# Kernel optimization log

Hardware: AMD Instinct MI355X
Metric: run time of the kernel (lower is better)

## Reference

```python
import jax, jax.numpy as jnp
import numpy as np

# Static block configuration (HTSAT stage-1 Swin block)
H = W = 64      # input_resolution
WS = 8          # window_size
SS = 4          # shift_size (window_size // 2)
NH = 4          # num_heads
C = 96          # dim
N = WS * WS     # tokens per window


def _rel_pos_index(ws):
    # mirrors WindowAttention.__init__ relative_position_index construction
    coords = np.stack(np.meshgrid(np.arange(ws), np.arange(ws), indexing='ij')).reshape(2, -1)
    rel = (coords[:, :, None] - coords[:, None, :]).transpose(1, 2, 0)
    rel[:, :, 0] += ws - 1
    rel[:, :, 1] += ws - 1
    rel[:, :, 0] *= 2 * ws - 1
    return rel.sum(-1)  # (N, N) int


def _attn_mask(h, w, ws, ss):
    # mirrors SwinTransformerBlock shifted-window attn_mask construction
    img = np.zeros((h, w))
    slices = (slice(0, -ws), slice(-ws, -ss), slice(-ss, None))
    cnt = 0
    for hs in slices:
        for wsl in slices:
            img[hs, wsl] = cnt
            cnt += 1
    mw = img.reshape(h // ws, ws, w // ws, ws).transpose(0, 2, 1, 3).reshape(-1, ws * ws)
    diff = mw[:, None, :] - mw[:, :, None]  # (nW, N, N)
    return np.where(diff != 0, -100.0, 0.0).astype(np.float32)


_REL_IDX = jnp.asarray(_rel_pos_index(WS))          # (N, N)
_ATTN_MASK = jnp.asarray(_attn_mask(H, W, WS, SS))  # (nW, N, N)


def _layernorm(x, g, b, eps=1e-5):
    mu = x.mean(-1, keepdims=True)
    var = ((x - mu) ** 2).mean(-1, keepdims=True)
    return (x - mu) * jax.lax.rsqrt(var + eps) * g + b


def setup_inputs() -> dict:
    key = jax.random.key(0)
    ks = jax.random.split(key, 6)
    B = 64
    std = 0.02
    return {
        'x': jax.random.normal(ks[0], (B, H * W, C), jnp.float32),
        'norm1_g': jnp.ones((C,), jnp.float32),
        'norm1_b': jnp.zeros((C,), jnp.float32),
        'qkv_w': jax.random.normal(ks[1], (3 * C, C), jnp.float32) * std,
        'qkv_b': jnp.zeros((3 * C,), jnp.float32),
        'rpb_table': jax.random.normal(ks[2], ((2 * WS - 1) ** 2, NH), jnp.float32) * std,
        'proj_w': jax.random.normal(ks[3], (C, C), jnp.float32) * std,
        'proj_b': jnp.zeros((C,), jnp.float32),
        'norm2_g': jnp.ones((C,), jnp.float32),
        'norm2_b': jnp.zeros((C,), jnp.float32),
        'fc1_w': jax.random.normal(ks[4], (4 * C, C), jnp.float32) * std,
        'fc1_b': jnp.zeros((4 * C,), jnp.float32),
        'fc2_w': jax.random.normal(ks[5], (C, 4 * C), jnp.float32) * std,
        'fc2_b': jnp.zeros((C,), jnp.float32),
    }


def reference(x, norm1_g, norm1_b, qkv_w, qkv_b, rpb_table, proj_w, proj_b,
              norm2_g, norm2_b, fc1_w, fc1_b, fc2_w, fc2_b):
    B, L, _ = x.shape
    hd = C // NH
    scale = hd ** (-0.5)

    shortcut = x
    h = _layernorm(x, norm1_g, norm1_b).reshape(B, H, W, C)
    # cyclic shift
    h = jnp.roll(h, (-SS, -SS), axis=(1, 2))
    # window partition -> (B*nW, N, C)
    hw = h.reshape(B, H // WS, WS, W // WS, WS, C).transpose(0, 1, 3, 2, 4, 5).reshape(-1, N, C)
    B_ = hw.shape[0]

    qkv = (hw @ qkv_w.T + qkv_b).reshape(B_, N, 3, NH, hd).transpose(2, 0, 3, 1, 4)
    q, k, v = qkv[0], qkv[1], qkv[2]  # (B_, NH, N, hd)

    attn = jnp.einsum('bhnd,bhmd->bhnm', q * scale, k)
    bias = rpb_table[_REL_IDX.reshape(-1)].reshape(N, N, NH).transpose(2, 0, 1)
    attn = attn + bias[None]
    nW = _ATTN_MASK.shape[0]
    attn = attn.reshape(B_ // nW, nW, NH, N, N) + _ATTN_MASK[None, :, None]
    attn = jax.nn.softmax(attn.reshape(B_, NH, N, N), axis=-1)

    o = jnp.einsum('bhnm,bhmd->bhnd', attn, v).transpose(0, 2, 1, 3).reshape(B_, N, C)
    o = o @ proj_w.T + proj_b
    # window reverse
    o = o.reshape(B, H // WS, W // WS, WS, WS, C).transpose(0, 1, 3, 2, 4, 5).reshape(B, H, W, C)
    o = jnp.roll(o, (SS, SS), axis=(1, 2))

    x = shortcut + o.reshape(B, L, C)
    h2 = _layernorm(x, norm2_g, norm2_b)
    h2 = jax.nn.gelu(h2 @ fc1_w.T + fc1_b, approximate=False) @ fc2_w.T + fc2_b
    return x + h2
```

## Files before the change

### kernel.cpp

```cpp
#include <hip/hip_runtime.h>
#include <math.h>

#define B_IMG 64
#define H_ 64
#define W_ 64
#define L_ (H_*W_)
#define C_ 96
#define WSZ 8
#define SSZ 4
#define NH_ 4
#define HD_ 24
#define NT_ 64

#define QKVW_OFF 0
#define PROJW_OFF 27648
#define W1_OFF   36864
#define W2_OFF   73728
#define WTOT     110592

typedef short bf16x8 __attribute__((ext_vector_type(8)));
typedef float f32x4  __attribute__((ext_vector_type(4)));

__device__ __forceinline__ float bf2f(unsigned short u) {
    union { unsigned int i; float f; } c; c.i = ((unsigned int)u) << 16; return c.f;
}
__device__ __forceinline__ unsigned short f2bf(float f) {
    union { float f; unsigned int i; } c; c.f = f;
    return (unsigned short)((c.i + 0x7fffu + ((c.i >> 16) & 1u)) >> 16);
}
__device__ __forceinline__ int reg_of(int ii, int jj, int whi, int wwi) {
    const int rh = (whi == 7) ? ((ii < SSZ) ? 1 : 2) : 0;
    const int rw = (wwi == 7) ? ((jj < SSZ) ? 1 : 2) : 0;
    return rh*3 + rw;
}

__global__ void k_conv(const float* __restrict__ qkvw, const float* __restrict__ projw,
                       const float* __restrict__ w1, const float* __restrict__ w2,
                       unsigned short* __restrict__ ws16) {
    int i = blockIdx.x * 256 + threadIdx.x;
    if (i >= WTOT) return;
    float v;
    if (i < PROJW_OFF)      v = qkvw[i];
    else if (i < W1_OFF)    v = projw[i - PROJW_OFF];
    else if (i < W2_OFF)    v = w1[i - W1_OFF];
    else                    v = w2[i - W2_OFF];
    ws16[i] = f2bf(v);
}

__global__ __launch_bounds__(256)
void k_attn(const float* __restrict__ x,
            const float* __restrict__ g1, const float* __restrict__ b1,
            const unsigned short* __restrict__ wsw,
            const float* __restrict__ qkvb,
            const float* __restrict__ rpbt,
            const float* __restrict__ projb,
            float* __restrict__ xmid)
{
    const int wid = blockIdx.x;
    const int b = wid >> 6, whi = (wid >> 3) & 7, wwi = wid & 7;
    const int tid = threadIdx.x;
    const int l = tid & 63, wv = tid >> 6;
    const int e = l & 15, g = l >> 4;

    __shared__ __align__(16) unsigned short hbn[NT_][104];
    __shared__ __align__(16) unsigned short qkps[NH_][4096];
    __shared__ __align__(16) unsigned short vt[NH_][2048];
    __shared__ float rpbf[900];

    {
        uint4* z = (uint4*)&qkps[0][0];
        for (int i = tid; i < 2048; i += 256) z[i] = (uint4){0,0,0,0};
        for (int i = tid; i < 900; i += 256) rpbf[i] = rpbt[i];
    }

    {
        const int tok = tid >> 2, q = tid & 3;
        const int i = tok >> 3, j = tok & 7;
        const int sr = (whi*WSZ + i + SSZ) & (H_-1);
        const int sc = (wwi*WSZ + j + SSZ) & (W_-1);
        const float* row = x + ((size_t)b*L_ + sr*W_ + sc) * C_;
        float v[24];
        float s = 0.f, s2 = 0.f;
#pragma unroll
        for (int m = 0; m < 6; ++m) {
            float4 f = ((const float4*)row)[q + 4*m];
            v[4*m+0]=f.x; v[4*m+1]=f.y; v[4*m+2]=f.z; v[4*m+3]=f.w;
            s  += f.x+f.y+f.z+f.w;
            s2 += f.x*f.x+f.y*f.y+f.z*f.z+f.w*f.w;
        }
        s  += __shfl_xor(s, 1);  s  += __shfl_xor(s, 2);
        s2 += __shfl_xor(s2, 1); s2 += __shfl_xor(s2, 2);
        const float mu = s * (1.f/96.f);
        const float rstd = rsqrtf(s2*(1.f/96.f) - mu*mu + 1e-5f);
#pragma unroll
        for (int m = 0; m < 6; ++m) {
            const int c0 = 4*(q + 4*m);
            float o0 = (v[4*m+0]-mu)*rstd*g1[c0+0] + b1[c0+0];
            float o1 = (v[4*m+1]-mu)*rstd*g1[c0+1] + b1[c0+1];
            float o2 = (v[4*m+2]-mu)*rstd*g1[c0+2] + b1[c0+2];
            float o3 = (v[4*m+3]-mu)*rstd*g1[c0+3] + b1[c0+3];
            uint2 u;
            u.x = (unsigned int)f2bf(o0) | ((unsigned int)f2bf(o1) << 16);
            u.y = (unsigned int)f2bf(o2) | ((unsigned int)f2bf(o3) << 16);
            *(uint2*)&hbn[tok][c0] = u;
        }
    }
    __syncthreads();

    {
        f32x4 acc[18];
#pragma unroll
        for (int nt = 0; nt < 18; ++nt) acc[nt] = (f32x4){0.f,0.f,0.f,0.f};
#pragma unroll
        for (int ks = 0; ks < 3; ++ks) {
            bf16x8 a = *(const bf16x8*)&hbn[wv*16 + e][ks*32 + g*8];
#pragma unroll
            for (int nt = 0; nt < 18; ++nt) {
                bf16x8 bw = *(const bf16x8*)(wsw + QKVW_OFF + (size_t)(nt*16 + e)*96 + ks*32 + g*8);
                acc[nt] = __builtin_amdgcn_mfma_f32_16x16x32_bf16(a, bw, acc[nt], 0, 0, 0);
            }
        }
#pragma unroll
        for (int nt = 0; nt < 18; ++nt) {
            const int col = nt*16 + e;
            const int seg = nt / 6;
            const int cs  = col - seg*96;
            const int hh  = cs / 24;
            const int dd  = cs - hh*24;
            const float bias = qkvb[col];
#pragma unroll
            for (int i = 0; i < 4; ++i) {
                const int row = wv*16 + g*4 + i;
                const float val = acc[nt][i] + bias;
                if (seg == 0)      qkps[hh][row*32 + dd] = f2bf(val * 0.20412414523193154f);
                else if (seg == 1) qkps[hh][2048 + row*32 + dd] = f2bf(val);
                else               vt[hh][dd*64 + ((((row*2) ^ ((dd&7)<<4))) >> 1)] = f2bf(val);
            }
        }
    }
    __syncthreads();

    {
        const int hd = wv;
        const unsigned short* qbase = &qkps[hd][0];
        const unsigned short* kbase = &qkps[hd][2048];
        unsigned short* psb = &qkps[hd][0];

        f32x4 acc[4][4];
        {
            bf16x8 qf[4], kf[4];
#pragma unroll
            for (int mt = 0; mt < 4; ++mt)
                qf[mt] = *(const bf16x8*)(qbase + (mt*16 + e)*32 + g*8);
#pragma unroll
            for (int nt = 0; nt < 4; ++nt)
                kf[nt] = *(const bf16x8*)(kbase + (nt*16 + e)*32 + g*8);
            const f32x4 zz = (f32x4){0.f,0.f,0.f,0.f};
#pragma unroll
            for (int mt = 0; mt < 4; ++mt)
#pragma unroll
                for (int nt = 0; nt < 4; ++nt)
                    acc[mt][nt] = __builtin_amdgcn_mfma_f32_16x16x32_bf16(qf[mt], kf[nt], zz, 0, 0, 0);
        }

        const int j2 = e & 7, i2b = e >> 3;
        int rgc[4];
#pragma unroll
        for (int nt = 0; nt < 4; ++nt) rgc[nt] = reg_of(nt*2 + i2b, j2, whi, wwi);

#pragma unroll
        for (int mt = 0; mt < 4; ++mt) {
#pragma unroll
            for (int ii = 0; ii < 4; ++ii) {
                const int r  = mt*16 + g*4 + ii;
                const int i1 = r >> 3, j1 = r & 7;
                const int rg1 = reg_of(i1, j1, whi, wwi);
                const int cbase = ((i1 + 7 - i2b)*15 + (j1 - j2 + 7))*4 + hd;
                float sv[4];
#pragma unroll
                for (int nt = 0; nt < 4; ++nt) {
                    float t = acc[mt][nt][ii] + rpbf[cbase - nt*120];
                    if (rg1 != rgc[nt]) t -= 100.f;
                    sv[nt] = t;
                }
                float m = fmaxf(fmaxf(sv[0], sv[1]), fmaxf(sv[2], sv[3]));
                m = fmaxf(m, __shfl_xor(m, 1)); m = fmaxf(m, __shfl_xor(m, 2));
                m = fmaxf(m, __shfl_xor(m, 4)); m = fmaxf(m, __shfl_xor(m, 8));
                float sum = 0.f;
#pragma unroll
                for (int nt = 0; nt < 4; ++nt) { sv[nt] = __expf(sv[nt] - m); sum += sv[nt]; }
                sum += __shfl_xor(sum, 1); sum += __shfl_xor(sum, 2);
                sum += __shfl_xor(sum, 4); sum += __shfl_xor(sum, 8);
                const float inv = 1.f / sum;
                const int swx = (r & 7) << 4;
#pragma unroll
                for (int nt = 0; nt < 4; ++nt) {
                    const int cbyte = (nt*16 + e)*2;
                    psb[r*64 + ((cbyte ^ swx) >> 1)] = f2bf(sv[nt] * inv);
                }
            }
        }
        asm volatile("s_waitcnt lgkmcnt(0)" ::: "memory");

        f32x4 acc2[4][2];
#pragma unroll
        for (int mt = 0; mt < 4; ++mt)
#pragma unroll
            for (int nt2 = 0; nt2 < 2; ++nt2) acc2[mt][nt2] = (f32x4){0.f,0.f,0.f,0.f};
#pragma unroll
        for (int ks2 = 0; ks2 < 2; ++ks2) {
            bf16x8 pf[4], vf[2];
#pragma unroll
            for (int mt = 0; mt < 4; ++mt) {
                const int rr = mt*16 + e;
                const int gg = (ks2*4 + g) ^ (rr & 7);
                pf[mt] = *(const bf16x8*)(psb + rr*64 + gg*8);
            }
#pragma unroll
            for (int nt2 = 0; nt2 < 2; ++nt2) {
                const int d = nt2*16 + e;
                const int gg = (ks2*4 + g) ^ (d & 7);
                vf[nt2] = *(const bf16x8*)(&vt[hd][0] + d*64 + gg*8);
            }
#pragma unroll
            for (int mt = 0; mt < 4; ++mt)
#pragma unroll
                for (int nt2 = 0; nt2 < 2; ++nt2)
                    acc2[mt][nt2] = __builtin_amdgcn_mfma_f32_16x16x32_bf16(pf[mt], vf[nt2], acc2[mt][nt2], 0, 0, 0);
        }
#pragma unroll
        for (int mt = 0; mt < 4; ++mt) {
#pragma unroll
            for (int ii = 0; ii < 4; ++ii) {
                const int r = mt*16 + g*4 + ii;
                hbn[r][hd*24 + e] = f2bf(acc2[mt][0][ii]);
                if (e < 8) hbn[r][hd*24 + 16 + e] = f2bf(acc2[mt][1][ii]);
            }
        }
    }
    __syncthreads();

    {
        f32x4 pacc[6];
#pragma unroll
        for (int nt = 0; nt < 6; ++nt) pacc[nt] = (f32x4){0.f,0.f,0.f,0.f};
#pragma unroll
        for (int ks = 0; ks < 3; ++ks) {
            bf16x8 a = *(const bf16x8*)&hbn[wv*16 + e][ks*32 + g*8];
#pragma unroll
            for (int nt = 0; nt < 6; ++nt) {
                bf16x8 bw = *(const bf16x8*)(wsw + PROJW_OFF + (size_t)(nt*16 + e)*96 + ks*32 + g*8);
                pacc[nt] = __builtin_amdgcn_mfma_f32_16x16x32_bf16(a, bw, pacc[nt], 0, 0, 0);
            }
        }
#pragma unroll
        for (int i = 0; i < 4; ++i) {
            const int n = wv*16 + g*4 + i;
            const int wi = n >> 3, wj = n & 7;
            const int sr = (whi*WSZ + wi + SSZ) & (H_-1);
            const int sc = (wwi*WSZ + wj + SSZ) & (W_-1);
            const size_t base = ((size_t)b*L_ + sr*W_ + sc)*C_;
#pragma unroll
            for (int nt = 0; nt < 6; ++nt) {
                const int c = nt*16 + e;
                xmid[base + c] = pacc[nt][i] + projb[c] + x[base + c];
            }
        }
    }
}

__global__ __launch_bounds__(256)
void k_mlp(float* xio,
           const float* __restrict__ g2, const float* __restrict__ b2,
           const unsigned short* __restrict__ wsw,
           const float* __restrict__ bb1, const float* __restrict__ bb2)
{
    const int r0 = blockIdx.x * 64;
    const int tid = threadIdx.x;
    const int l = tid & 63, wv = tid >> 6;
    const int lr = l & 15, lk = l >> 4;

    __shared__ __align__(16) unsigned short hbn[64][120];
    __shared__ __align__(16) unsigned short h1s[64][392];

    {
        const int rr = tid >> 2, q = tid & 3;
        const float* row = xio + (size_t)(r0+rr)*C_;
        float v[24];
        float s = 0.f, s2 = 0.f;
#pragma unroll
        for (int m = 0; m < 6; ++m) {
            float4 f = ((const float4*)row)[q + 4*m];
            v[4*m+0]=f.x; v[4*m+1]=f.y; v[4*m+2]=f.z; v[4*m+3]=f.w;
            s  += f.x+f.y+f.z+f.w;
            s2 += f.x*f.x+f.y*f.y+f.z*f.z+f.w*f.w;
        }
        s  += __shfl_xor(s, 1);  s  += __shfl_xor(s, 2);
        s2 += __shfl_xor(s2, 1); s2 += __shfl_xor(s2, 2);
        const float mu = s * (1.f/96.f);
        const float rstd = rsqrtf(s2*(1.f/96.f) - mu*mu + 1e-5f);
#pragma unroll
        for (int m = 0; m < 6; ++m) {
            const int c0 = 4*(q + 4*m);
            float o0 = (v[4*m+0]-mu)*rstd*g2[c0+0] + b2[c0+0];
            float o1 = (v[4*m+1]-mu)*rstd*g2[c0+1] + b2[c0+1];
            float o2 = (v[4*m+2]-mu)*rstd*g2[c0+2] + b2[c0+2];
            float o3 = (v[4*m+3]-mu)*rstd*g2[c0+3] + b2[c0+3];
            uint2 u;
            u.x = (unsigned int)f2bf(o0) | ((unsigned int)f2bf(o1) << 16);
            u.y = (unsigned int)f2bf(o2) | ((unsigned int)f2bf(o3) << 16);
            *(uint2*)&hbn[rr][c0] = u;
        }
    }
    __syncthreads();

#pragma unroll
    for (int half = 0; half < 2; ++half) {
        f32x4 acc[12];
#pragma unroll
        for (int t = 0; t < 12; ++t) acc[t] = (f32x4){0.f,0.f,0.f,0.f};
#pragma unroll
        for (int ks = 0; ks < 3; ++ks) {
            bf16x8 a = *(const bf16x8*)&hbn[wv*16 + lr][ks*32 + lk*8];
#pragma unroll
            for (int nt = 0; nt < 12; ++nt) {
                bf16x8 bf = *(const bf16x8*)(wsw + W1_OFF + (size_t)(half*192 + nt*16 + lr)*96 + ks*32 + lk*8);
                acc[nt] = __builtin_amdgcn_mfma_f32_16x16x32_bf16(a, bf, acc[nt], 0, 0, 0);
            }
        }
#pragma unroll
        for (int nt = 0; nt < 12; ++nt) {
            const int col = half*192 + nt*16 + lr;
            const float bias = bb1[col];
#pragma unroll
            for (int i = 0; i < 4; ++i) {
                const int rrow = wv*16 + lk*4 + i;
                const float t = acc[nt][i] + bias;
                h1s[rrow][col] = f2bf(0.5f*t*(1.f + erff(t*0.70710678118654752f)));
            }
        }
    }
    __syncthreads();

    {
        f32x4 acc[6];
#pragma unroll
        for (int t = 0; t < 6; ++t) acc[t] = (f32x4){0.f,0.f,0.f,0.f};
#pragma unroll
        for (int ks = 0; ks < 12; ++ks) {
            bf16x8 a = *(const bf16x8*)&h1s[wv*16 + lr][ks*32 + lk*8];
#pragma unroll
            for (int nt = 0; nt < 6; ++nt) {
                bf16x8 bf = *(const bf16x8*)(wsw + W2_OFF + (size_t)(nt*16 + lr)*384 + ks*32 + lk*8);
                acc[nt] = __builtin_amdgcn_mfma_f32_16x16x32_bf16(a, bf, acc[nt], 0, 0, 0);
            }
        }
#pragma unroll
        for (int nt = 0; nt < 6; ++nt) {
            const int col = nt*16 + lr;
            const float bias = bb2[col];
#pragma unroll
            for (int i = 0; i < 4; ++i) {
                const int row = r0 + wv*16 + lk*4 + i;
                float* p = xio + (size_t)row*C_ + col;
                *p = acc[nt][i] + bias + *p;
            }
        }
    }
}

extern "C" void kernel_launch(void* const* d_in, const int* in_sizes, int n_in,
                              void* d_out, int out_size, void* d_ws, size_t ws_size,
                              hipStream_t stream) {
    const float* x    = (const float*)d_in[0];
    const float* n1g  = (const float*)d_in[1];
    const float* n1b  = (const float*)d_in[2];
    const float* qkvw = (const float*)d_in[3];
    const float* qkvb = (const float*)d_in[4];
    const float* rpbt = (const float*)d_in[5];
    const float* pw   = (const float*)d_in[6];
    const float* pb   = (const float*)d_in[7];
    const float* n2g  = (const float*)d_in[8];
    const float* n2b  = (const float*)d_in[9];
    const float* w1   = (const float*)d_in[10];
    const float* b1f  = (const float*)d_in[11];
    const float* w2   = (const float*)d_in[12];
    const float* b2f  = (const float*)d_in[13];
    float* outp = (float*)d_out;
    unsigned short* wsw = (unsigned short*)d_ws;

    k_conv<<<dim3((WTOT + 255)/256), dim3(256), 0, stream>>>(qkvw, pw, w1, w2, wsw);
    k_attn<<<dim3(4096), dim3(256), 0, stream>>>(x, n1g, n1b, wsw, qkvb, rpbt, pb, outp);
    k_mlp <<<dim3(4096), dim3(256), 0, stream>>>(outp, n2g, n2b, wsw, b1f, b2f);
}
```

Before: 606.9 us.

## Use 512-thread blocks splitting GEMM column tiles across eight waves

Both fused kernels move from 4 to 8 waves per block. The extra waves split the N dimension of the QKV, projection, fc1 and fc2 GEMMs and the query rows of attention, and layernorm uses 8 threads per token. The aim is fewer accumulator registers per wave and more waves in flight to hide latency from global weight loads. The cost is an added barrier in attention so Q/K fragments are read before P overwrites them, plus more scheduling and barrier overhead per block.

```diff
diff --git a/kernel.cpp b/kernel.cpp
--- a/kernel.cpp
+++ b/kernel.cpp
@@ -47,7 +47,7 @@
     ws16[i] = f2bf(v);
 }
 
-__global__ __launch_bounds__(256)
+__global__ __launch_bounds__(512)
 void k_attn(const float* __restrict__ x,
             const float* __restrict__ g1, const float* __restrict__ b1,
             const unsigned short* __restrict__ wsw,
@@ -69,32 +69,32 @@
 
     {
         uint4* z = (uint4*)&qkps[0][0];
-        for (int i = tid; i < 2048; i += 256) z[i] = (uint4){0,0,0,0};
-        for (int i = tid; i < 900; i += 256) rpbf[i] = rpbt[i];
-    }
-
-    {
-        const int tok = tid >> 2, q = tid & 3;
+        for (int i = tid; i < 2048; i += 512) z[i] = (uint4){0,0,0,0};
+        for (int i = tid; i < 900; i += 512) rpbf[i] = rpbt[i];
+    }
+
+    {
+        const int tok = tid >> 3, q = tid & 7;
         const int i = tok >> 3, j = tok & 7;
         const int sr = (whi*WSZ + i + SSZ) & (H_-1);
         const int sc = (wwi*WSZ + j + SSZ) & (W_-1);
         const float* row = x + ((size_t)b*L_ + sr*W_ + sc) * C_;
-        float v[24];
+        float v[12];
         float s = 0.f, s2 = 0.f;
 #pragma unroll
-        for (int m = 0; m < 6; ++m) {
-            float4 f = ((const float4*)row)[q + 4*m];
+        for (int m = 0; m < 3; ++m) {
+            float4 f = ((const float4*)row)[q + 8*m];
             v[4*m+0]=f.x; v[4*m+1]=f.y; v[4*m+2]=f.z; v[4*m+3]=f.w;
             s  += f.x+f.y+f.z+f.w;
             s2 += f.x*f.x+f.y*f.y+f.z*f.z+f.w*f.w;
         }
-        s  += __shfl_xor(s, 1);  s  += __shfl_xor(s, 2);
-        s2 += __shfl_xor(s2, 1); s2 += __shfl_xor(s2, 2);
+        s  += __shfl_xor(s, 1);  s  += __shfl_xor(s, 2);  s  += __shfl_xor(s, 4);
+        s2 += __shfl_xor(s2, 1); s2 += __shfl_xor(s2, 2); s2 += __shfl_xor(s2, 4);
         const float mu = s * (1.f/96.f);
         const float rstd = rsqrtf(s2*(1.f/96.f) - mu*mu + 1e-5f);
 #pragma unroll
-        for (int m = 0; m < 6; ++m) {
-            const int c0 = 4*(q + 4*m);
+        for (int m = 0; m < 3; ++m) {
+            const int c0 = 4*(q + 8*m);
             float o0 = (v[4*m+0]-mu)*rstd*g1[c0+0] + b1[c0+0];
             float o1 = (v[4*m+1]-mu)*rstd*g1[c0+1] + b1[c0+1];
             float o2 = (v[4*m+2]-mu)*rstd*g1[c0+2] + b1[c0+2];
@@ -108,20 +108,22 @@
     __syncthreads();
 
     {
-        f32x4 acc[18];
-#pragma unroll
-        for (int nt = 0; nt < 18; ++nt) acc[nt] = (f32x4){0.f,0.f,0.f,0.f};
+        const int mt = wv & 3, nbase = (wv >> 2) * 9;
+        f32x4 acc[9];
+#pragma unroll
+        for (int nt = 0; nt < 9; ++nt) acc[nt] = (f32x4){0.f,0.f,0.f,0.f};
 #pragma unroll
         for (int ks = 0; ks < 3; ++ks) {
-            bf16x8 a = *(const bf16x8*)&hbn[wv*16 + e][ks*32 + g*8];
-#pragma unroll
-            for (int nt = 0; nt < 18; ++nt) {
-                bf16x8 bw = *(const bf16x8*)(wsw + QKVW_OFF + (size_t)(nt*16 + e)*96 + ks*32 + g*8);
-                acc[nt] = __builtin_amdgcn_mfma_f32_16x16x32_bf16(a, bw, acc[nt], 0, 0, 0);
-            }
-        }
-#pragma unroll
-        for (int nt = 0; nt < 18; ++nt) {
+            bf16x8 a = *(const bf16x8*)&hbn[mt*16 + e][ks*32 + g*8];
+#pragma unroll
+            for (int ntl = 0; ntl < 9; ++ntl) {
+                bf16x8 bw = *(const bf16x8*)(wsw + QKVW_OFF + (size_t)((nbase+ntl)*16 + e)*96 + ks*32 + g*8);
+                acc[ntl] = __builtin_amdgcn_mfma_f32_16x16x32_bf16(a, bw, acc[ntl], 0, 0, 0);
+            }
+        }
+#pragma unroll
+        for (int ntl = 0; ntl < 9; ++ntl) {
+            const int nt = nbase + ntl;
             const int col = nt*16 + e;
             const int seg = nt / 6;
             const int cs  = col - seg*96;
@@ -130,8 +132,8 @@
             const float bias = qkvb[col];
 #pragma unroll
             for (int i = 0; i < 4; ++i) {
-                const int row = wv*16 + g*4 + i;
-                const float val = acc[nt][i] + bias;
+                const int row = mt*16 + g*4 + i;
+                const float val = acc[ntl][i] + bias;
                 if (seg == 0)      qkps[hh][row*32 + dd] = f2bf(val * 0.20412414523193154f);
                 else if (seg == 1) qkps[hh][2048 + row*32 + dd] = f2bf(val);
                 else               vt[hh][dd*64 + ((((row*2) ^ ((dd&7)<<4))) >> 1)] = f2bf(val);
@@ -141,26 +143,30 @@
     __syncthreads();
 
     {
-        const int hd = wv;
+        const int hd = wv & 3, mhalf = wv >> 2;
         const unsigned short* qbase = &qkps[hd][0];
         const unsigned short* kbase = &qkps[hd][2048];
         unsigned short* psb = &qkps[hd][0];
 
-        f32x4 acc[4][4];
+        bf16x8 qf[2], kf[4];
+#pragma unroll
+        for (int mtl = 0; mtl < 2; ++mtl) {
+            const int mt = mhalf*2 + mtl;
+            qf[mtl] = *(const bf16x8*)(qbase + (mt*16 + e)*32 + g*8);
+        }
+#pragma unroll
+        for (int nt = 0; nt < 4; ++nt)
+            kf[nt] = *(const bf16x8*)(kbase + (nt*16 + e)*32 + g*8);
+        __syncthreads();
+
+        f32x4 acc[2][4];
         {
-            bf16x8 qf[4], kf[4];
-#pragma unroll
-            for (int mt = 0; mt < 4; ++mt)
-                qf[mt] = *(const bf16x8*)(qbase + (mt*16 + e)*32 + g*8);
-#pragma unroll
-            for (int nt = 0; nt < 4; ++nt)
-                kf[nt] = *(const bf16x8*)(kbase + (nt*16 + e)*32 + g*8);
             const f32x4 zz = (f32x4){0.f,0.f,0.f,0.f};
 #pragma unroll
-            for (int mt = 0; mt < 4; ++mt)
+            for (int mtl = 0; mtl < 2; ++mtl)
 #pragma unroll
                 for (int nt = 0; nt < 4; ++nt)
-                    acc[mt][nt] = __builtin_amdgcn_mfma_f32_16x16x32_bf16(qf[mt], kf[nt], zz, 0, 0, 0);
+                    acc[mtl][nt] = __builtin_amdgcn_mfma_f32_16x16x32_bf16(qf[mtl], kf[nt], zz, 0, 0, 0);
         }
 
         const int j2 = e & 7, i2b = e >> 3;
@@ -169,17 +175,17 @@
         for (int nt = 0; nt < 4; ++nt) rgc[nt] = reg_of(nt*2 + i2b, j2, whi, wwi);
 
 #pragma unroll
-        for (int mt = 0; mt < 4; ++mt) {
+        for (int mtl = 0; mtl < 2; ++mtl) {
 #pragma unroll
             for (int ii = 0; ii < 4; ++ii) {
-                const int r  = mt*16 + g*4 + ii;
+                const int r  = (mhalf*2 + mtl)*16 + g*4 + ii;
                 const int i1 = r >> 3, j1 = r & 7;
                 const int rg1 = reg_of(i1, j1, whi, wwi);
                 const int cbase = ((i1 + 7 - i2b)*15 + (j1 - j2 + 7))*4 + hd;
                 float sv[4];
 #pragma unroll
                 for (int nt = 0; nt < 4; ++nt) {
-                    float t = acc[mt][nt][ii] + rpbf[cbase - nt*120];
+                    float t = acc[mtl][nt][ii] + rpbf[cbase - nt*120];
                     if (rg1 != rgc[nt]) t -= 100.f;
                     sv[nt] = t;
                 }
@@ -202,19 +208,19 @@
         }
         asm volatile("s_waitcnt lgkmcnt(0)" ::: "memory");
 
-        f32x4 acc2[4][2];
-#pragma unroll
-        for (int mt = 0; mt < 4; ++mt)
-#pragma unroll
-            for (int nt2 = 0; nt2 < 2; ++nt2) acc2[mt][nt2] = (f32x4){0.f,0.f,0.f,0.f};
+        f32x4 acc2[2][2];
+#pragma unroll
+        for (int mtl = 0; mtl < 2; ++mtl)
+#pragma unroll
+            for (int nt2 = 0; nt2 < 2; ++nt2) acc2[mtl][nt2] = (f32x4){0.f,0.f,0.f,0.f};
 #pragma unroll
         for (int ks2 = 0; ks2 < 2; ++ks2) {
-            bf16x8 pf[4], vf[2];
-#pragma unroll
-            for (int mt = 0; mt < 4; ++mt) {
-                const int rr = mt*16 + e;
+            bf16x8 pf[2], vf[2];
+#pragma unroll
+            for (int mtl = 0; mtl < 2; ++mtl) {
+                const int rr = (mhalf*2 + mtl)*16 + e;
                 const int gg = (ks2*4 + g) ^ (rr & 7);
-                pf[mt] = *(const bf16x8*)(psb + rr*64 + gg*8);
+                pf[mtl] = *(const bf16x8*)(psb + rr*64 + gg*8);
             }
 #pragma unroll
             for (int nt2 = 0; nt2 < 2; ++nt2) {
@@ -223,53 +229,55 @@
                 vf[nt2] = *(const bf16x8*)(&vt[hd][0] + d*64 + gg*8);
             }
 #pragma unroll
-            for (int mt = 0; mt < 4; ++mt)
+            for (int mtl = 0; mtl < 2; ++mtl)
 #pragma unroll
                 for (int nt2 = 0; nt2 < 2; ++nt2)
-                    acc2[mt][nt2] = __builtin_amdgcn_mfma_f32_16x16x32_bf16(pf[mt], vf[nt2], acc2[mt][nt2], 0, 0, 0);
-        }
-#pragma unroll
-        for (int mt = 0; mt < 4; ++mt) {
+                    acc2[mtl][nt2] = __builtin_amdgcn_mfma_f32_16x16x32_bf16(pf[mtl], vf[nt2], acc2[mtl][nt2], 0, 0, 0);
+        }
+#pragma unroll
+        for (int mtl = 0; mtl < 2; ++mtl) {
 #pragma unroll
             for (int ii = 0; ii < 4; ++ii) {
-                const int r = mt*16 + g*4 + ii;
-                hbn[r][hd*24 + e] = f2bf(acc2[mt][0][ii]);
-                if (e < 8) hbn[r][hd*24 + 16 + e] = f2bf(acc2[mt][1][ii]);
+                const int r = (mhalf*2 + mtl)*16 + g*4 + ii;
+                hbn[r][hd*24 + e] = f2bf(acc2[mtl][0][ii]);
+                if (e < 8) hbn[r][hd*24 + 16 + e] = f2bf(acc2[mtl][1][ii]);
             }
         }
     }
     __syncthreads();
 
     {
-        f32x4 pacc[6];
-#pragma unroll
-        for (int nt = 0; nt < 6; ++nt) pacc[nt] = (f32x4){0.f,0.f,0.f,0.f};
+        const int mt = wv & 3, nh = wv >> 2;
+        f32x4 pacc[3];
+#pragma unroll
+        for (int nt = 0; nt < 3; ++nt) pacc[nt] = (f32x4){0.f,0.f,0.f,0.f};
 #pragma unroll
         for (int ks = 0; ks < 3; ++ks) {
-            bf16x8 a = *(const bf16x8*)&hbn[wv*16 + e][ks*32 + g*8];
-#pragma unroll
-            for (int nt = 0; nt < 6; ++nt) {
-                bf16x8 bw = *(const bf16x8*)(wsw + PROJW_OFF + (size_t)(nt*16 + e)*96 + ks*32 + g*8);
+            bf16x8 a = *(const bf16x8*)&hbn[mt*16 + e][ks*32 + g*8];
+#pragma unroll
+            for (int nt = 0; nt < 3; ++nt) {
+                const int col = nh*48 + nt*16 + e;
+                bf16x8 bw = *(const bf16x8*)(wsw + PROJW_OFF + (size_t)col*96 + ks*32 + g*8);
                 pacc[nt] = __builtin_amdgcn_mfma_f32_16x16x32_bf16(a, bw, pacc[nt], 0, 0, 0);
             }
         }
 #pragma unroll
         for (int i = 0; i < 4; ++i) {
-            const int n = wv*16 + g*4 + i;
+            const int n = mt*16 + g*4 + i;
             const int wi = n >> 3, wj = n & 7;
             const int sr = (whi*WSZ + wi + SSZ) & (H_-1);
             const int sc = (wwi*WSZ + wj + SSZ) & (W_-1);
             const size_t base = ((size_t)b*L_ + sr*W_ + sc)*C_;
 #pragma unroll
-            for (int nt = 0; nt < 6; ++nt) {
-                const int c = nt*16 + e;
+            for (int nt = 0; nt < 3; ++nt) {
+                const int c = nh*48 + nt*16 + e;
                 xmid[base + c] = pacc[nt][i] + projb[c] + x[base + c];
             }
         }
     }
 }
 
-__global__ __launch_bounds__(256)
+__global__ __launch_bounds__(512)
 void k_mlp(float* xio,
            const float* __restrict__ g2, const float* __restrict__ b2,
            const unsigned short* __restrict__ wsw,
@@ -284,24 +292,24 @@
     __shared__ __align__(16) unsigned short h1s[64][392];
 
     {
-        const int rr = tid >> 2, q = tid & 3;
+        const int rr = tid >> 3, q = tid & 7;
         const float* row = xio + (size_t)(r0+rr)*C_;
-        float v[24];
+        float v[12];
         float s = 0.f, s2 = 0.f;
 #pragma unroll
-        for (int m = 0; m < 6; ++m) {
-            float4 f = ((const float4*)row)[q + 4*m];
+        for (int m = 0; m < 3; ++m) {
+            float4 f = ((const float4*)row)[q + 8*m];
             v[4*m+0]=f.x; v[4*m+1]=f.y; v[4*m+2]=f.z; v[4*m+3]=f.w;
             s  += f.x+f.y+f.z+f.w;
             s2 += f.x*f.x+f.y*f.y+f.z*f.z+f.w*f.w;
         }
-        s  += __shfl_xor(s, 1);  s  += __shfl_xor(s, 2);
-        s2 += __shfl_xor(s2, 1); s2 += __shfl_xor(s2, 2);
+        s  += __shfl_xor(s, 1);  s  += __shfl_xor(s, 2);  s  += __shfl_xor(s, 4);
+        s2 += __shfl_xor(s2, 1); s2 += __shfl_xor(s2, 2); s2 += __shfl_xor(s2, 4);
         const float mu = s * (1.f/96.f);
         const float rstd = rsqrtf(s2*(1.f/96.f) - mu*mu + 1e-5f);
 #pragma unroll
-        for (int m = 0; m < 6; ++m) {
-            const int c0 = 4*(q + 4*m);
+        for (int m = 0; m < 3; ++m) {
+            const int c0 = 4*(q + 8*m);
             float o0 = (v[4*m+0]-mu)*rstd*g2[c0+0] + b2[c0+0];
             float o1 = (v[4*m+1]-mu)*rstd*g2[c0+1] + b2[c0+1];
             float o2 = (v[4*m+2]-mu)*rstd*g2[c0+2] + b2[c0+2];
@@ -314,27 +322,28 @@
     }
     __syncthreads();
 
-#pragma unroll
-    for (int half = 0; half < 2; ++half) {
+    {
+        const int mt = wv & 3, nh = wv >> 2;
         f32x4 acc[12];
 #pragma unroll
         for (int t = 0; t < 12; ++t) acc[t] = (f32x4){0.f,0.f,0.f,0.f};
 #pragma unroll
         for (int ks = 0; ks < 3; ++ks) {
-            bf16x8 a = *(const bf16x8*)&hbn[wv*16 + lr][ks*32 + lk*8];
+            bf16x8 a = *(const bf16x8*)&hbn[mt*16 + lr][ks*32 + lk*8];
 #pragma unroll
             for (int nt = 0; nt < 12; ++nt) {
-                bf16x8 bf = *(const bf16x8*)(wsw + W1_OFF + (size_t)(half*192 + nt*16 + lr)*96 + ks*32 + lk*8);
+                const int col = nh*192 + nt*16 + lr;
+                bf16x8 bf = *(const bf16x8*)(wsw + W1_OFF + (size_t)col*96 + ks*32 + lk*8);
                 acc[nt] = __builtin_amdgcn_mfma_f32_16x16x32_bf16(a, bf, acc[nt], 0, 0, 0);
             }
         }
 #pragma unroll
         for (int nt = 0; nt < 12; ++nt) {
-            const int col = half*192 + nt*16 + lr;
+            const int col = nh*192 + nt*16 + lr;
             const float bias = bb1[col];
 #pragma unroll
             for (int i = 0; i < 4; ++i) {
-                const int rrow = wv*16 + lk*4 + i;
+                const int rrow = mt*16 + lk*4 + i;
                 const float t = acc[nt][i] + bias;
                 h1s[rrow][col] = f2bf(0.5f*t*(1.f + erff(t*0.70710678118654752f)));
             }
@@ -343,25 +352,27 @@
     __syncthreads();
 
     {
-        f32x4 acc[6];
-#pragma unroll
-        for (int t = 0; t < 6; ++t) acc[t] = (f32x4){0.f,0.f,0.f,0.f};
+        const int mt = wv & 3, nh = wv >> 2;
+        f32x4 acc[3];
+#pragma unroll
+        for (int t = 0; t < 3; ++t) acc[t] = (f32x4){0.f,0.f,0.f,0.f};
 #pragma unroll
         for (int ks = 0; ks < 12; ++ks) {
-            bf16x8 a = *(const bf16x8*)&h1s[wv*16 + lr][ks*32 + lk*8];
-#pragma unroll
-            for (int nt = 0; nt < 6; ++nt) {
-                bf16x8 bf = *(const bf16x8*)(wsw + W2_OFF + (size_t)(nt*16 + lr)*384 + ks*32 + lk*8);
+            bf16x8 a = *(const bf16x8*)&h1s[mt*16 + lr][ks*32 + lk*8];
+#pragma unroll
+            for (int nt = 0; nt < 3; ++nt) {
+                const int col = nh*48 + nt*16 + lr;
+                bf16x8 bf = *(const bf16x8*)(wsw + W2_OFF + (size_t)col*384 + ks*32 + lk*8);
                 acc[nt] = __builtin_amdgcn_mfma_f32_16x16x32_bf16(a, bf, acc[nt], 0, 0, 0);
             }
         }
 #pragma unroll
-        for (int nt = 0; nt < 6; ++nt) {
-            const int col = nt*16 + lr;
+        for (int nt = 0; nt < 3; ++nt) {
+            const int col = nh*48 + nt*16 + lr;
             const float bias = bb2[col];
 #pragma unroll
             for (int i = 0; i < 4; ++i) {
-                const int row = r0 + wv*16 + lk*4 + i;
+                const int row = r0 + mt*16 + lk*4 + i;
                 float* p = xio + (size_t)row*C_ + col;
                 *p = acc[nt][i] + bias + *p;
             }
@@ -390,6 +401,6 @@
     unsigned short* wsw = (unsigned short*)d_ws;
 
     k_conv<<<dim3((WTOT + 255)/256), dim3(256), 0, stream>>>(qkvw, pw, w1, w2, wsw);
-    k_attn<<<dim3(4096), dim3(256), 0, stream>>>(x, n1g, n1b, wsw, qkvb, rpbt, pb, outp);
-    k_mlp <<<dim3(4096), dim3(256), 0, stream>>>(outp, n2g, n2b, wsw, b1f, b2f);
-}
+    k_attn<<<dim3(4096), dim3(512), 0, stream>>>(x, n1g, n1b, wsw, qkvb, rpbt, pb, outp);
+    k_mlp <<<dim3(4096), dim3(512), 0, stream>>>(outp, n2g, n2b, wsw, b1f, b2f);
+}
```

Measured after the change: 546.8 us. -9.9%, faster.
